# Optimization experiments

Hardware: AMD Instinct MI355X
Metric: run time of the kernel (lower is better)

Reference implementation:

```python
import jax, jax.numpy as jnp
import numpy as np

N_USERS = 100000
M_ITEMS = 50000
D = 64
NNZ = 4_000_000
B = 4096
LAYERS = 3


def setup_inputs() -> dict:
    key = jax.random.key(0)
    ks = jax.random.split(key, 7)
    N = N_USERS + M_ITEMS
    return {
        "users": jax.random.randint(ks[0], (B,), 0, N_USERS, dtype=jnp.int64 if jax.config.jax_enable_x64 else jnp.int32),
        "items": jax.random.randint(ks[1], (B,), 0, M_ITEMS, dtype=jnp.int64 if jax.config.jax_enable_x64 else jnp.int32),
        "user_emb": jax.random.normal(ks[2], (N_USERS, D), dtype=jnp.float32) * 0.1,
        "item_emb": jax.random.normal(ks[3], (M_ITEMS, D), dtype=jnp.float32) * 0.1,
        "adj_rows": jax.random.randint(ks[4], (NNZ,), 0, N, dtype=jnp.int32),
        "adj_cols": jax.random.randint(ks[5], (NNZ,), 0, N, dtype=jnp.int32),
        "adj_vals": jax.random.uniform(ks[6], (NNZ,), dtype=jnp.float32),
    }


def reference(users, items, user_emb, item_emb, adj_rows, adj_cols, adj_vals):
    n_users = user_emb.shape[0]
    N = n_users + item_emb.shape[0]

    # computer(): multi-layer sparse propagation, mean over layer outputs
    all_emb = jnp.concatenate([user_emb, item_emb], axis=0)  # [N, D]
    acc = all_emb
    emb = all_emb
    for _ in range(LAYERS):
        # SpMM as gather + segment-sum: (A @ emb)[r] = sum_{e: row(e)=r} val(e) * emb[col(e)]
        messages = adj_vals[:, None] * emb[adj_cols]          # [NNZ, D]
        emb = jax.ops.segment_sum(messages, adj_rows, num_segments=N)
        acc = acc + emb
    light_out = acc / (LAYERS + 1)                            # mean over stacked layers

    all_users = light_out[:n_users]
    all_items = light_out[n_users:]

    # forward(users, items)
    u = all_users[users]                                      # [B, D]
    i = all_items[items]                                      # [B, D]
    gamma = jnp.sum(u * i, axis=1)                            # [B]
    return gamma
```

## Files before the change

kernel.cpp:

```cpp
#include <hip/hip_runtime.h>

#define N_USERS 100000
#define M_ITEMS 50000
#define N_TOTAL (N_USERS + M_ITEMS)
#define D 64
#define NNZ 4000000
#define BATCH 4096

#define RPB 128
#define BSHIFT 7
#define NBUCKETS ((N_TOTAL + RPB - 1) / RPB)
#define BCAP 7680

#define TILE 8192
#define SCAT_BLOCKS ((NNZ + TILE - 1) / TILE)
#define SCAT_THREADS 1024
#define EPT (TILE / SCAT_THREADS)
#define CPB 2

#define LS_THREADS 1024
#define LS_EPT 8

typedef __attribute__((ext_vector_type(2))) float f32x2;

__device__ __forceinline__ unsigned pack_bf16(float a, float b) {
    unsigned ua = __float_as_uint(a);
    unsigned ub = __float_as_uint(b);
    ua = (ua + 0x7FFFu + ((ua >> 16) & 1u)) >> 16;
    ub = (ub + 0x7FFFu + ((ub >> 16) & 1u)) & 0xFFFF0000u;
    return ua | ub;
}
__device__ __forceinline__ float bf16_lo(unsigned p) { return __uint_as_float(p << 16); }
__device__ __forceinline__ float bf16_hi(unsigned p) { return __uint_as_float(p & 0xFFFF0000u); }

__device__ __forceinline__ f32x2 unpack_bf16x2(unsigned p) {
    union { unsigned u[2]; f32x2 f; } r;
    r.u[0] = p << 16;
    r.u[1] = p & 0xFFFF0000u;
    return r.f;
}


__global__ void init_emb_kernel(const float4* __restrict__ ue,
                                const float4* __restrict__ ie,
                                uint2* __restrict__ emb) {
    size_t i = (size_t)blockIdx.x * blockDim.x + threadIdx.x;
    const size_t nu4  = (size_t)N_USERS * D / 4;
    const size_t tot4 = (size_t)N_TOTAL * D / 4;
    if (i >= tot4) return;
    float4 f = (i < nu4) ? ue[i] : ie[i - nu4];
    emb[i] = make_uint2(pack_bf16(f.x, f.y), pack_bf16(f.z, f.w));
}

__global__ void init_acc_kernel(const int* __restrict__ users,
                                const int* __restrict__ items,
                                const float* __restrict__ ue,
                                const float* __restrict__ ie,
                                float* __restrict__ u_acc,
                                float* __restrict__ i_acc) {
    int gid = blockIdx.x * blockDim.x + threadIdx.x;
    int d = gid & (D - 1);
    int b = gid >> 6;
    if (b < BATCH) {
        u_acc[(size_t)b * D + d] = ue[(size_t)users[b] * D + d];
    } else if (b < 2 * BATCH) {
        int bb = b - BATCH;
        i_acc[(size_t)bb * D + d] = ie[(size_t)items[bb] * D + d];
    }
}


__global__ void bucket_hist_kernel(const int* __restrict__ rows,
                                   int* __restrict__ bucketcnt) {
    __shared__ int h[NBUCKETS];
    for (int i = threadIdx.x; i < NBUCKETS; i += blockDim.x) h[i] = 0;
    __syncthreads();
    int stride = gridDim.x * blockDim.x;
    for (int e = blockIdx.x * blockDim.x + threadIdx.x; e < NNZ; e += stride)
        atomicAdd(&h[rows[e] >> BSHIFT], 1);
    __syncthreads();
    for (int i = threadIdx.x; i < NBUCKETS; i += blockDim.x)
        if (h[i]) atomicAdd(&bucketcnt[i], h[i]);
}

__global__ void bucket_scan_kernel(const int* __restrict__ cnt,
                                   int* __restrict__ bucketoff,
                                   int* __restrict__ cursor) {
    __shared__ int sc[1024];
    int t = threadIdx.x;
    int i0 = t * 2, i1 = t * 2 + 1;
    int a = (i0 < NBUCKETS) ? cnt[i0] : 0;
    int b = (i1 < NBUCKETS) ? cnt[i1] : 0;
    sc[t] = a + b;
    __syncthreads();
    for (int o = 1; o < 1024; o <<= 1) {
        int v = (t >= o) ? sc[t - o] : 0;
        __syncthreads();
        sc[t] += v;
        __syncthreads();
    }
    int excl = (t == 0) ? 0 : sc[t - 1];
    if (i0 < NBUCKETS) { bucketoff[i0] = excl;     cursor[i0] = excl; }
    if (i1 < NBUCKETS) { bucketoff[i1] = excl + a; cursor[i1] = excl + a; }
    if (t == 0) bucketoff[NBUCKETS] = NNZ;
}

__global__ __launch_bounds__(SCAT_THREADS)
void bucket_scatter_kernel(const int* __restrict__ rows,
                           const int* __restrict__ cols,
                           const float* __restrict__ vals,
                           int* __restrict__ cursor,
                           int2* __restrict__ bucketed) {
    __shared__ int hist[NBUCKETS];
    __shared__ int loff[NBUCKETS + 1];
    __shared__ int partial[SCAT_THREADS];
    __shared__ int2 buf[TILE];
    __shared__ int dst[TILE];
    int t = threadIdx.x;
    size_t start = (size_t)blockIdx.x * TILE;
    int n = (int)(((size_t)NNZ - start < TILE) ? ((size_t)NNZ - start) : TILE);

    for (int i = t; i < NBUCKETS; i += SCAT_THREADS) hist[i] = 0;
    __syncthreads();
    int rowv[EPT];
    int rank[EPT];
#pragma unroll
    for (int k = 0; k < EPT; ++k) {
        int i = t + k * SCAT_THREADS;
        if (i < n) {
            int r = rows[start + i];
            rowv[k] = r;
            rank[k] = atomicAdd(&hist[r >> BSHIFT], 1);
        }
    }
    __syncthreads();
    {
        int base = t * CPB;
        int s = 0;
#pragma unroll
        for (int j = 0; j < CPB; ++j) {
            int idx = base + j;
            if (idx < NBUCKETS) s += hist[idx];
        }
        partial[t] = s;
        __syncthreads();
        for (int o = 1; o < SCAT_THREADS; o <<= 1) {
            int v = (t >= o) ? partial[t - o] : 0;
            __syncthreads();
            partial[t] += v;
            __syncthreads();
        }
        int excl = (t == 0) ? 0 : partial[t - 1];
#pragma unroll
        for (int j = 0; j < CPB; ++j) {
            int idx = base + j;
            if (idx < NBUCKETS) { loff[idx] = excl; excl += hist[idx]; }
        }
        if (t == 0) loff[NBUCKETS] = n;
    }
    __syncthreads();
    for (int i = t; i < NBUCKETS; i += SCAT_THREADS) {
        int c = loff[i + 1] - loff[i];
        hist[i] = c ? atomicAdd(&cursor[i], c) : 0;
    }
    __syncthreads();
#pragma unroll
    for (int k = 0; k < EPT; ++k) {
        int i = t + k * SCAT_THREADS;
        if (i < n) {
            int r = rowv[k];
            int bkt = r >> BSHIFT;
            int slot = loff[bkt] + rank[k];
            buf[slot] = make_int2(((r & (RPB - 1)) << 18) | cols[start + i],
                                  __float_as_int(vals[start + i]));
            dst[slot] = hist[bkt] + rank[k];
        }
    }
    __syncthreads();
    for (int i = t; i < n; i += SCAT_THREADS)
        bucketed[dst[i]] = buf[i];
}

__global__ __launch_bounds__(LS_THREADS)
void local_sort_kernel(const int* __restrict__ bucketoff,
                       const int2* __restrict__ bucketed,
                       int* __restrict__ row_start,
                       int2* __restrict__ edges) {
    __shared__ int hist[RPB];
    __shared__ int sc[RPB];
    __shared__ int2 buf[BCAP];
    int b = blockIdx.x;
    int t = threadIdx.x;
    int s = bucketoff[b], e = bucketoff[b + 1], n = e - s;

    if (t < RPB) hist[t] = 0;
    __syncthreads();
    int rl[LS_EPT], rank[LS_EPT];
    int2 pay[LS_EPT];
#pragma unroll
    for (int k = 0; k < LS_EPT; ++k) {
        int i = t + k * LS_THREADS;
        if (i < n) {
            int2 ev = bucketed[s + i];
            rl[k] = (int)((unsigned)ev.x >> 18);
            pay[k] = make_int2((ev.x & 0x3FFFF) << 7, ev.y);
            rank[k] = atomicAdd(&hist[rl[k]], 1);
        }
    }
    __syncthreads();
    if (t < RPB) sc[t] = hist[t];
    __syncthreads();
    for (int o = 1; o < RPB; o <<= 1) {
        int v = (t < RPB && t >= o) ? sc[t - o] : 0;
        __syncthreads();
        if (t < RPB) sc[t] += v;
        __syncthreads();
    }
    if (t < RPB) {
        int excl = (t == 0) ? 0 : sc[t - 1];
        int gr = b * RPB + t;
        if (gr < N_TOTAL) row_start[gr] = s + excl;
    }
    if (b == 0 && t == 0) row_start[N_TOTAL] = NNZ;
    __syncthreads();
#pragma unroll
    for (int k = 0; k < LS_EPT; ++k) {
        int i = t + k * LS_THREADS;
        if (i < n) {
            int excl = (rl[k] == 0) ? 0 : sc[rl[k] - 1];
            int p = excl + rank[k];
            if (p < BCAP) buf[p] = pay[k];
            else          edges[s + p] = pay[k];
        }
    }
    __syncthreads();
    int m = (n < BCAP) ? n : BCAP;
    for (int i = t; i < m; i += LS_THREADS) edges[s + i] = buf[i];
}


#define EDGE_SLOT(ei, ji)                                                    \
    {                                                                        \
        int   c_  = (ji < n) ? ei.x : 0;                                     \
        float mv_ = (ji < n) ? __int_as_float(ei.y) : 0.0f;                  \
        uint4 p_  = *(const uint4*)(ebase + c_);                             \
        f32x2 vv_ = {mv_, mv_};                                              \
        a01 = __builtin_elementwise_fma(unpack_bf16x2(p_.x), vv_, a01);      \
        a23 = __builtin_elementwise_fma(unpack_bf16x2(p_.y), vv_, a23);      \
        a45 = __builtin_elementwise_fma(unpack_bf16x2(p_.z), vv_, a45);      \
        a67 = __builtin_elementwise_fma(unpack_bf16x2(p_.w), vv_, a67);      \
    }

#define SPMM_BODY(row_s, row_e)                                              \
    int n = (row_e) - (row_s);                                               \
    const int2* ep = edges + (row_s) + oct;                                  \
    f32x2 a01 = {0.f, 0.f}, a23 = {0.f, 0.f};                                \
    f32x2 a45 = {0.f, 0.f}, a67 = {0.f, 0.f};                                \
    int tmax = (n + 7) >> 3;                                                 \
    int t = 0;                                                               \
    for (; t + 4 <= tmax; t += 4) {                                          \
        int2 e0 = ep[0], e1 = ep[8], e2 = ep[16], e3 = ep[24];               \
        ep += 32;                                                            \
        int j0 = (t << 3) + oct;                                             \
        EDGE_SLOT(e0, j0);                                                   \
        EDGE_SLOT(e1, (j0 + 8));                                             \
        EDGE_SLOT(e2, (j0 + 16));                                            \
        EDGE_SLOT(e3, (j0 + 24));                                            \
    }                                                                        \
    if (t + 2 <= tmax) {                                                     \
        int2 e0 = ep[0], e1 = ep[8];                                         \
        ep += 16;                                                            \
        int j0 = (t << 3) + oct;                                             \
        EDGE_SLOT(e0, j0);                                                   \
        EDGE_SLOT(e1, (j0 + 8));                                             \
        t += 2;                                                              \
    }                                                                        \
    if (t < tmax) {                                                          \
        int2 e0 = ep[0];                                                     \
        int j0 = (t << 3) + oct;                                             \
        EDGE_SLOT(e0, j0);                                                   \
    }                                                                        \
    _Pragma("unroll")                                                        \
    for (int o = 8; o <= 32; o <<= 1) {                                      \
        a01.x += __shfl_xor(a01.x, o, 64); a01.y += __shfl_xor(a01.y, o, 64);\
        a23.x += __shfl_xor(a23.x, o, 64); a23.y += __shfl_xor(a23.y, o, 64);\
        a45.x += __shfl_xor(a45.x, o, 64); a45.y += __shfl_xor(a45.y, o, 64);\
        a67.x += __shfl_xor(a67.x, o, 64); a67.y += __shfl_xor(a67.y, o, 64);\
    }

__global__ void spmm_csr_kernel(const int* __restrict__ row_start,
                                const int2* __restrict__ edges,
                                const char* __restrict__ emb_in,
                                uint4* __restrict__ emb_out) {
    int wave = (blockIdx.x * blockDim.x + threadIdx.x) >> 6;
    int lane = threadIdx.x & 63;
    if (wave >= N_TOTAL) return;
    int oct = lane >> 3;
    int ui  = lane & 7;
    const char* ebase = emb_in + (ui << 4);
    int s = row_start[wave];
    int e = row_start[wave + 1];
    SPMM_BODY(s, e);
    if (oct == 0)
        emb_out[(size_t)wave * 8 + ui] =
            make_uint4(pack_bf16(a01.x, a01.y), pack_bf16(a23.x, a23.y),
                       pack_bf16(a45.x, a45.y), pack_bf16(a67.x, a67.y));
}

__global__ void layer3_kernel(const int* __restrict__ users,
                              const int* __restrict__ items,
                              const int* __restrict__ row_start,
                              const int2* __restrict__ edges,
                              const char* __restrict__ emb_in,
                              float* __restrict__ u_acc,
                              float* __restrict__ i_acc) {
    int wave = (blockIdx.x * blockDim.x + threadIdx.x) >> 6;
    int lane = threadIdx.x & 63;
    if (wave >= 2 * BATCH) return;
    int oct = lane >> 3;
    int ui  = lane & 7;
    const char* ebase = emb_in + (ui << 4);
    int row;
    float* dstp;
    if (wave < BATCH) {
        row = users[wave];
        dstp = &u_acc[(size_t)wave * D];
    } else {
        int bb = wave - BATCH;
        row = N_USERS + items[bb];
        dstp = &i_acc[(size_t)bb * D];
    }
    int s = row_start[row];
    int e = row_start[row + 1];
    SPMM_BODY(s, e);
    if (oct == 0) {
        dstp[8 * ui + 0] += a01.x; dstp[8 * ui + 1] += a01.y;
        dstp[8 * ui + 2] += a23.x; dstp[8 * ui + 3] += a23.y;
        dstp[8 * ui + 4] += a45.x; dstp[8 * ui + 5] += a45.y;
        dstp[8 * ui + 6] += a67.x; dstp[8 * ui + 7] += a67.y;
    }
}

__global__ void gather_acc_kernel(const int* __restrict__ users,
                                  const int* __restrict__ items,
                                  const unsigned* __restrict__ emb,
                                  float* __restrict__ u_acc,
                                  float* __restrict__ i_acc) {
    int gid = blockIdx.x * blockDim.x + threadIdx.x;
    int ui = gid & 31;
    int b  = gid >> 5;
    if (b < BATCH) {
        unsigned p = emb[(size_t)users[b] * 32 + ui];
        u_acc[(size_t)b * D + 2 * ui]     += bf16_lo(p);
        u_acc[(size_t)b * D + 2 * ui + 1] += bf16_hi(p);
    } else if (b < 2 * BATCH) {
        int bb = b - BATCH;
        unsigned p = emb[((size_t)(N_USERS + items[bb])) * 32 + ui];
        i_acc[(size_t)bb * D + 2 * ui]     += bf16_lo(p);
        i_acc[(size_t)bb * D + 2 * ui + 1] += bf16_hi(p);
    }
}

__global__ void final_dot_kernel(const float* __restrict__ u_acc,
                                 const float* __restrict__ i_acc,
                                 float* __restrict__ out) {
    int gid = blockIdx.x * blockDim.x + threadIdx.x;
    int b = gid >> 6;
    int lane = gid & 63;
    if (b >= BATCH) return;
    float p = u_acc[(size_t)b * D + lane] * i_acc[(size_t)b * D + lane];
#pragma unroll
    for (int o = 32; o; o >>= 1) p += __shfl_xor(p, o, 64);
    if (lane == 0) out[b] = p * (1.0f / 16.0f);
}


extern "C" void kernel_launch(void* const* d_in, const int* in_sizes, int n_in,
                              void* d_out, int out_size, void* d_ws, size_t ws_size,
                              hipStream_t stream) {
    const int*   users = (const int*)d_in[0];
    const int*   items = (const int*)d_in[1];
    const float* ue    = (const float*)d_in[2];
    const float* ie    = (const float*)d_in[3];
    const int*   rows  = (const int*)d_in[4];
    const int*   cols  = (const int*)d_in[5];
    const float* vals  = (const float*)d_in[6];
    float*       out   = (float*)d_out;

    char* ws = (char*)d_ws;
    size_t off = 0;
    auto alloc = [&](size_t bytes) {
        void* p = ws + off;
        off += (bytes + 255) & ~(size_t)255;
        return p;
    };
    const size_t NBH = (size_t)N_TOTAL * D * sizeof(unsigned short);
    char*  embA      = (char*)alloc(NBH);
    char*  embB      = (char*)alloc(NBH);
    float* u_acc     = (float*)alloc((size_t)BATCH * D * sizeof(float));
    float* i_acc     = (float*)alloc((size_t)BATCH * D * sizeof(float));
    int*   row_start = (int*)alloc(((size_t)N_TOTAL + 1) * sizeof(int));
    int*   bucketcnt = (int*)alloc((size_t)NBUCKETS * sizeof(int));
    int*   bucketoff = (int*)alloc(((size_t)NBUCKETS + 1) * sizeof(int));
    int*   cursor    = (int*)alloc((size_t)NBUCKETS * sizeof(int));
    int2*  edges     = (int2*)alloc((size_t)NNZ * sizeof(int2) + 256);
    int2*  bucketed  = (int2*)alloc((size_t)NNZ * sizeof(int2));

    {
        size_t tot4 = (size_t)N_TOTAL * D / 4;
        init_emb_kernel<<<(unsigned)((tot4 + 255) / 256), 256, 0, stream>>>(
            (const float4*)ue, (const float4*)ie, (uint2*)embA);
        init_acc_kernel<<<(2 * BATCH * D + 255) / 256, 256, 0, stream>>>(
            users, items, ue, ie, u_acc, i_acc);
    }

    hipMemsetAsync(bucketcnt, 0, (size_t)NBUCKETS * sizeof(int), stream);
    bucket_hist_kernel<<<512, 256, 0, stream>>>(rows, bucketcnt);
    bucket_scan_kernel<<<1, 1024, 0, stream>>>(bucketcnt, bucketoff, cursor);
    bucket_scatter_kernel<<<SCAT_BLOCKS, SCAT_THREADS, 0, stream>>>(
        rows, cols, vals, cursor, bucketed);
    local_sort_kernel<<<NBUCKETS, LS_THREADS, 0, stream>>>(
        bucketoff, bucketed, row_start, edges);

    spmm_csr_kernel<<<(N_TOTAL * 64 + 255) / 256, 256, 0, stream>>>(
        row_start, edges, embA, (uint4*)embB);
    gather_acc_kernel<<<(2 * BATCH * 32 + 255) / 256, 256, 0, stream>>>(
        users, items, (const unsigned*)embB, u_acc, i_acc);

    spmm_csr_kernel<<<(N_TOTAL * 64 + 255) / 256, 256, 0, stream>>>(
        row_start, edges, embB, (uint4*)embA);
    gather_acc_kernel<<<(2 * BATCH * 32 + 255) / 256, 256, 0, stream>>>(
        users, items, (const unsigned*)embA, u_acc, i_acc);

    layer3_kernel<<<(2 * BATCH * 64 + 255) / 256, 256, 0, stream>>>(
        users, items, row_start, edges, embA, u_acc, i_acc);

    final_dot_kernel<<<(BATCH * 64 + 255) / 256, 256, 0, stream>>>(u_acc, i_acc, out);
}
```

Measured before the change: 351.7 us.

## Fuse batch accumulation, layer-3 SpMM and dot into one kernel; nontemporal loads

Replaces the init_acc, two gather_acc, layer3 and final_dot kernels with one finalize kernel. For each batch pair it computes layer-3 rows in registers, adds the original and layer 1/2 embeddings read directly, and reduces the dot product, so the u_acc/i_acc buffers are no longer read and written repeatedly. This removes four kernel launches and that accumulator traffic. It also switches streaming reads of rows/cols/vals, bucketed and edges to nontemporal loads to reduce cache pollution, at the risk of losing cache reuse where edges are read again by the later SpMM passes.

```diff
diff --git a/kernel.cpp b/kernel.cpp
--- a/kernel.cpp
+++ b/kernel.cpp
@@ -22,6 +22,7 @@
 #define LS_EPT 8
 
 typedef __attribute__((ext_vector_type(2))) float f32x2;
+typedef __attribute__((ext_vector_type(2))) int   i32x2;
 
 __device__ __forceinline__ unsigned pack_bf16(float a, float b) {
     unsigned ua = __float_as_uint(a);
@@ -52,23 +53,6 @@
     emb[i] = make_uint2(pack_bf16(f.x, f.y), pack_bf16(f.z, f.w));
 }
 
-__global__ void init_acc_kernel(const int* __restrict__ users,
-                                const int* __restrict__ items,
-                                const float* __restrict__ ue,
-                                const float* __restrict__ ie,
-                                float* __restrict__ u_acc,
-                                float* __restrict__ i_acc) {
-    int gid = blockIdx.x * blockDim.x + threadIdx.x;
-    int d = gid & (D - 1);
-    int b = gid >> 6;
-    if (b < BATCH) {
-        u_acc[(size_t)b * D + d] = ue[(size_t)users[b] * D + d];
-    } else if (b < 2 * BATCH) {
-        int bb = b - BATCH;
-        i_acc[(size_t)bb * D + d] = ie[(size_t)items[bb] * D + d];
-    }
-}
-
 
 __global__ void bucket_hist_kernel(const int* __restrict__ rows,
                                    int* __restrict__ bucketcnt) {
@@ -77,7 +61,7 @@
     __syncthreads();
     int stride = gridDim.x * blockDim.x;
     for (int e = blockIdx.x * blockDim.x + threadIdx.x; e < NNZ; e += stride)
-        atomicAdd(&h[rows[e] >> BSHIFT], 1);
+        atomicAdd(&h[__builtin_nontemporal_load(rows + e) >> BSHIFT], 1);
     __syncthreads();
     for (int i = threadIdx.x; i < NBUCKETS; i += blockDim.x)
         if (h[i]) atomicAdd(&bucketcnt[i], h[i]);
@@ -128,7 +112,7 @@
     for (int k = 0; k < EPT; ++k) {
         int i = t + k * SCAT_THREADS;
         if (i < n) {
-            int r = rows[start + i];
+            int r = __builtin_nontemporal_load(rows + start + i);
             rowv[k] = r;
             rank[k] = atomicAdd(&hist[r >> BSHIFT], 1);
         }
@@ -171,8 +155,9 @@
             int r = rowv[k];
             int bkt = r >> BSHIFT;
             int slot = loff[bkt] + rank[k];
-            buf[slot] = make_int2(((r & (RPB - 1)) << 18) | cols[start + i],
-                                  __float_as_int(vals[start + i]));
+            int cv = __builtin_nontemporal_load(cols + start + i);
+            float vv = __builtin_nontemporal_load(vals + start + i);
+            buf[slot] = make_int2(((r & (RPB - 1)) << 18) | cv, __float_as_int(vv));
             dst[slot] = hist[bkt] + rank[k];
         }
     }
@@ -201,7 +186,7 @@
     for (int k = 0; k < LS_EPT; ++k) {
         int i = t + k * LS_THREADS;
         if (i < n) {
-            int2 ev = bucketed[s + i];
+            i32x2 ev = __builtin_nontemporal_load((const i32x2*)(bucketed + s + i));
             rl[k] = (int)((unsigned)ev.x >> 18);
             pay[k] = make_int2((ev.x & 0x3FFFF) << 7, ev.y);
             rank[k] = atomicAdd(&hist[rl[k]], 1);
@@ -238,6 +223,8 @@
     for (int i = t; i < m; i += LS_THREADS) edges[s + i] = buf[i];
 }
 
+
+#define EDGE_LD(p_) __builtin_nontemporal_load((const i32x2*)(p_))
 
 #define EDGE_SLOT(ei, ji)                                                    \
     {                                                                        \
@@ -259,7 +246,8 @@
     int tmax = (n + 7) >> 3;                                                 \
     int t = 0;                                                               \
     for (; t + 4 <= tmax; t += 4) {                                          \
-        int2 e0 = ep[0], e1 = ep[8], e2 = ep[16], e3 = ep[24];               \
+        i32x2 e0 = EDGE_LD(ep), e1 = EDGE_LD(ep + 8);                        \
+        i32x2 e2 = EDGE_LD(ep + 16), e3 = EDGE_LD(ep + 24);                  \
         ep += 32;                                                            \
         int j0 = (t << 3) + oct;                                             \
         EDGE_SLOT(e0, j0);                                                   \
@@ -268,7 +256,7 @@
         EDGE_SLOT(e3, (j0 + 24));                                            \
     }                                                                        \
     if (t + 2 <= tmax) {                                                     \
-        int2 e0 = ep[0], e1 = ep[8];                                         \
+        i32x2 e0 = EDGE_LD(ep), e1 = EDGE_LD(ep + 8);                        \
         ep += 16;                                                            \
         int j0 = (t << 3) + oct;                                             \
         EDGE_SLOT(e0, j0);                                                   \
@@ -276,7 +264,7 @@
         t += 2;                                                              \
     }                                                                        \
     if (t < tmax) {                                                          \
-        int2 e0 = ep[0];                                                     \
+        i32x2 e0 = EDGE_LD(ep);                                              \
         int j0 = (t << 3) + oct;                                             \
         EDGE_SLOT(e0, j0);                                                   \
     }                                                                        \
@@ -307,71 +295,68 @@
                        pack_bf16(a45.x, a45.y), pack_bf16(a67.x, a67.y));
 }
 
-__global__ void layer3_kernel(const int* __restrict__ users,
-                              const int* __restrict__ items,
-                              const int* __restrict__ row_start,
-                              const int2* __restrict__ edges,
-                              const char* __restrict__ emb_in,
-                              float* __restrict__ u_acc,
-                              float* __restrict__ i_acc) {
+__global__ void finalize_kernel(const int* __restrict__ users,
+                                const int* __restrict__ items,
+                                const float* __restrict__ ue,
+                                const float* __restrict__ ie,
+                                const int* __restrict__ row_start,
+                                const int2* __restrict__ edges,
+                                const char* __restrict__ embB,
+                                const char* __restrict__ embA,
+                                float* __restrict__ out) {
     int wave = (blockIdx.x * blockDim.x + threadIdx.x) >> 6;
     int lane = threadIdx.x & 63;
-    if (wave >= 2 * BATCH) return;
+    if (wave >= BATCH) return;
     int oct = lane >> 3;
     int ui  = lane & 7;
-    const char* ebase = emb_in + (ui << 4);
-    int row;
-    float* dstp;
-    if (wave < BATCH) {
-        row = users[wave];
-        dstp = &u_acc[(size_t)wave * D];
-    } else {
-        int bb = wave - BATCH;
-        row = N_USERS + items[bb];
-        dstp = &i_acc[(size_t)bb * D];
-    }
-    int s = row_start[row];
-    int e = row_start[row + 1];
-    SPMM_BODY(s, e);
-    if (oct == 0) {
-        dstp[8 * ui + 0] += a01.x; dstp[8 * ui + 1] += a01.y;
-        dstp[8 * ui + 2] += a23.x; dstp[8 * ui + 3] += a23.y;
-        dstp[8 * ui + 4] += a45.x; dstp[8 * ui + 5] += a45.y;
-        dstp[8 * ui + 6] += a67.x; dstp[8 * ui + 7] += a67.y;
-    }
-}
-
-__global__ void gather_acc_kernel(const int* __restrict__ users,
-                                  const int* __restrict__ items,
-                                  const unsigned* __restrict__ emb,
-                                  float* __restrict__ u_acc,
-                                  float* __restrict__ i_acc) {
-    int gid = blockIdx.x * blockDim.x + threadIdx.x;
-    int ui = gid & 31;
-    int b  = gid >> 5;
-    if (b < BATCH) {
-        unsigned p = emb[(size_t)users[b] * 32 + ui];
-        u_acc[(size_t)b * D + 2 * ui]     += bf16_lo(p);
-        u_acc[(size_t)b * D + 2 * ui + 1] += bf16_hi(p);
-    } else if (b < 2 * BATCH) {
-        int bb = b - BATCH;
-        unsigned p = emb[((size_t)(N_USERS + items[bb])) * 32 + ui];
-        i_acc[(size_t)bb * D + 2 * ui]     += bf16_lo(p);
-        i_acc[(size_t)bb * D + 2 * ui + 1] += bf16_hi(p);
-    }
-}
-
-__global__ void final_dot_kernel(const float* __restrict__ u_acc,
-                                 const float* __restrict__ i_acc,
-                                 float* __restrict__ out) {
-    int gid = blockIdx.x * blockDim.x + threadIdx.x;
-    int b = gid >> 6;
-    int lane = gid & 63;
-    if (b >= BATCH) return;
-    float p = u_acc[(size_t)b * D + lane] * i_acc[(size_t)b * D + lane];
-#pragma unroll
-    for (int o = 32; o; o >>= 1) p += __shfl_xor(p, o, 64);
-    if (lane == 0) out[b] = p * (1.0f / 16.0f);
+    const char* ebase = embA + (ui << 4);
+
+    int ru = users[wave];
+    int ri = N_USERS + items[wave];
+
+    f32x2 u01, u23, u45, u67, i01, i23, i45, i67;
+    {
+        SPMM_BODY(row_start[ru], row_start[ru + 1]);
+        u01 = a01; u23 = a23; u45 = a45; u67 = a67;
+    }
+    {
+        SPMM_BODY(row_start[ri], row_start[ri + 1]);
+        i01 = a01; i23 = a23; i45 = a45; i67 = a67;
+    }
+
+    {
+        const float4* up = (const float4*)(ue + (size_t)ru * D + 8 * ui);
+        float4 f0 = up[0], f1 = up[1];
+        u01 += (f32x2){f0.x, f0.y}; u23 += (f32x2){f0.z, f0.w};
+        u45 += (f32x2){f1.x, f1.y}; u67 += (f32x2){f1.z, f1.w};
+        uint4 pb = *(const uint4*)(embB + (size_t)ru * 128 + (ui << 4));
+        uint4 pa = *(const uint4*)(embA + (size_t)ru * 128 + (ui << 4));
+        u01 += unpack_bf16x2(pb.x) + unpack_bf16x2(pa.x);
+        u23 += unpack_bf16x2(pb.y) + unpack_bf16x2(pa.y);
+        u45 += unpack_bf16x2(pb.z) + unpack_bf16x2(pa.z);
+        u67 += unpack_bf16x2(pb.w) + unpack_bf16x2(pa.w);
+    }
+    {
+        const float4* ip = (const float4*)(ie + (size_t)items[wave] * D + 8 * ui);
+        float4 f0 = ip[0], f1 = ip[1];
+        i01 += (f32x2){f0.x, f0.y}; i23 += (f32x2){f0.z, f0.w};
+        i45 += (f32x2){f1.x, f1.y}; i67 += (f32x2){f1.z, f1.w};
+        uint4 pb = *(const uint4*)(embB + (size_t)ri * 128 + (ui << 4));
+        uint4 pa = *(const uint4*)(embA + (size_t)ri * 128 + (ui << 4));
+        i01 += unpack_bf16x2(pb.x) + unpack_bf16x2(pa.x);
+        i23 += unpack_bf16x2(pb.y) + unpack_bf16x2(pa.y);
+        i45 += unpack_bf16x2(pb.z) + unpack_bf16x2(pa.z);
+        i67 += unpack_bf16x2(pb.w) + unpack_bf16x2(pa.w);
+    }
+
+    f32x2 d = u01 * i01;
+    d = __builtin_elementwise_fma(u23, i23, d);
+    d = __builtin_elementwise_fma(u45, i45, d);
+    d = __builtin_elementwise_fma(u67, i67, d);
+    float p = d.x + d.y;
+#pragma unroll
+    for (int o = 1; o <= 4; o <<= 1) p += __shfl_xor(p, o, 64);
+    if (lane == 0) out[wave] = p * (1.0f / 16.0f);
 }
 
 
@@ -397,8 +382,6 @@
     const size_t NBH = (size_t)N_TOTAL * D * sizeof(unsigned short);
     char*  embA      = (char*)alloc(NBH);
     char*  embB      = (char*)alloc(NBH);
-    float* u_acc     = (float*)alloc((size_t)BATCH * D * sizeof(float));
-    float* i_acc     = (float*)alloc((size_t)BATCH * D * sizeof(float));
     int*   row_start = (int*)alloc(((size_t)N_TOTAL + 1) * sizeof(int));
     int*   bucketcnt = (int*)alloc((size_t)NBUCKETS * sizeof(int));
     int*   bucketoff = (int*)alloc(((size_t)NBUCKETS + 1) * sizeof(int));
@@ -410,8 +393,6 @@
         size_t tot4 = (size_t)N_TOTAL * D / 4;
         init_emb_kernel<<<(unsigned)((tot4 + 255) / 256), 256, 0, stream>>>(
             (const float4*)ue, (const float4*)ie, (uint2*)embA);
-        init_acc_kernel<<<(2 * BATCH * D + 255) / 256, 256, 0, stream>>>(
-            users, items, ue, ie, u_acc, i_acc);
     }
 
     hipMemsetAsync(bucketcnt, 0, (size_t)NBUCKETS * sizeof(int), stream);
@@ -424,16 +405,10 @@
 
     spmm_csr_kernel<<<(N_TOTAL * 64 + 255) / 256, 256, 0, stream>>>(
         row_start, edges, embA, (uint4*)embB);
-    gather_acc_kernel<<<(2 * BATCH * 32 + 255) / 256, 256, 0, stream>>>(
-        users, items, (const unsigned*)embB, u_acc, i_acc);
 
     spmm_csr_kernel<<<(N_TOTAL * 64 + 255) / 256, 256, 0, stream>>>(
         row_start, edges, embB, (uint4*)embA);
-    gather_acc_kernel<<<(2 * BATCH * 32 + 255) / 256, 256, 0, stream>>>(
-        users, items, (const unsigned*)embA, u_acc, i_acc);
-
-    layer3_kernel<<<(2 * BATCH * 64 + 255) / 256, 256, 0, stream>>>(
-        users, items, row_start, edges, embA, u_acc, i_acc);
-
-    final_dot_kernel<<<(BATCH * 64 + 255) / 256, 256, 0, stream>>>(u_acc, i_acc, out);
-}
+
+    finalize_kernel<<<(BATCH * 64 + 255) / 256, 256, 0, stream>>>(
+        users, items, ue, ie, row_start, edges, embB, embA, out);
+}
```

Result: faster. 344.1 us (-2.2%).
